# Kernel tuning notes

Hardware: AMD Instinct MI355X
Metric: run time of the kernel (lower is better)

Reference implementation:

```python
import math
import jax, jax.numpy as jnp
import numpy as np

HEAD_DIM = 64
N_HEAD = 8
INIT_SIZE = 1200  # -> 1201 embeddings, origin_shift = 601


def rel_sinusoidal_pos_embed(seq_len, dim=HEAD_DIM):
    """Matches RelativeSinusoidalPositionalEmbedding(dim, padding_idx=0, init_size=1200)."""
    num = INIT_SIZE + 1  # 1201
    half = dim // 2
    inv_freq = jnp.exp(jnp.arange(half, dtype=jnp.float32) * -(math.log(10000.0) / (half - 1)))
    pos = jnp.arange(-(num // 2), num // 2, dtype=jnp.float32)  # -601 .. 599 (1201 values)
    ang = pos[:, None] * inv_freq[None, :]                      # [num, half]
    w = jnp.concatenate([jnp.sin(ang), jnp.cos(ang)], axis=1)   # [num, dim]
    w = w.at[0].set(0.0)  # padding_idx row zeroed
    origin_shift = num // 2 + 1  # 601
    idx = jnp.arange(-seq_len, seq_len) + origin_shift          # [2L]
    return w[idx]                                               # [2L, dim]


def _shift(BD):
    # BD: [b, n, L, 2L] -> [b, n, L, L] (Transformer-XL skew trick)
    b, n, L, _ = BD.shape
    BD = jnp.pad(BD, ((0, 0), (0, 0), (0, 0), (0, 1)))  # [b,n,L,2L+1]
    BD = BD.reshape(b, n, 2 * L + 1, L)[:, :, :-1].reshape(b, n, L, 2 * L)
    return BD[:, :, :, L:]


def _transpose_shift(E):
    # E: [b, n, L, 2L] -> [b, n, L, L]
    b, n, L, _ = E.shape
    E = jnp.pad(E, ((0, 0), (0, 0), (0, 0), (0, 1))).reshape(b, n, 2 * L + 1, L)
    idx = jnp.arange(L) * 2 + 1
    return jnp.swapaxes(E[:, :, idx, :], -1, -2)


def setup_inputs() -> dict:
    key = jax.random.key(0)
    k1, k2, k3, k4 = jax.random.split(key, 4)
    B, L, D = 8, 512, 512
    x = jax.random.normal(k1, (B, L, D), dtype=jnp.float32)
    mask = jnp.ones((B, L), dtype=jnp.int32)
    W_qkv = jax.random.normal(k2, (D, 3 * D), dtype=jnp.float32) * (1.0 / math.sqrt(D))
    r_r_bias = jax.random.normal(k3, (N_HEAD, HEAD_DIM), dtype=jnp.float32) * 0.1
    r_w_bias = jax.random.normal(k4, (N_HEAD, HEAD_DIM), dtype=jnp.float32) * 0.1
    return {"x": x, "mask": mask, "W_qkv": W_qkv, "r_r_bias": r_r_bias, "r_w_bias": r_w_bias}


def reference(x, mask, W_qkv, r_r_bias, r_w_bias):
    B, L, D = x.shape
    scale = math.sqrt(HEAD_DIM)
    pos = rel_sinusoidal_pos_embed(L)  # [2L, head_dim], detached constant

    qkv = x @ W_qkv  # [B, L, 3D]
    q, k, v = jnp.split(qkv, 3, axis=-1)
    q = q.reshape(B, L, N_HEAD, HEAD_DIM).transpose(0, 2, 1, 3)  # [B,H,L,d]
    k = k.reshape(B, L, N_HEAD, HEAD_DIM).transpose(0, 2, 1, 3)
    v = v.reshape(B, L, N_HEAD, HEAD_DIM).transpose(0, 2, 1, 3)

    rw_head_q = q + r_r_bias[None, :, None, :]
    AC = jnp.einsum('bnqd,bnkd->bnqk', rw_head_q, k)              # [B,H,L,L]
    D_ = jnp.einsum('nd,ld->nl', r_w_bias, pos)[None, :, None, :] # [1,H,1,2L]
    B_ = jnp.einsum('bnqd,ld->bnql', q, pos)                      # [B,H,L,2L]
    E_ = jnp.einsum('bnqd,ld->bnql', k, pos)                      # [B,H,L,2L]

    BDE = _shift(B_ + D_) + _transpose_shift(E_)                  # [B,H,L,L]
    attn = (AC + BDE) / scale
    attn = jnp.where(mask[:, None, None, :] == 0, -jnp.inf, attn)
    attn = jax.nn.softmax(attn, axis=-1)

    out = jnp.matmul(attn, v)                                     # [B,H,L,d]
    return out.transpose(0, 2, 1, 3).reshape(B, L, D)
```

## Files before the change

kernel.cpp:

```cpp
#include <hip/hip_runtime.h>
#include <hip/hip_bf16.h>
#include <math.h>

#define LSEQ 512
#define DDIM 192

typedef __attribute__((ext_vector_type(8))) short s16x8;
typedef __attribute__((ext_vector_type(4))) float f32x4;
typedef unsigned short ushort_t;
typedef unsigned int uint_t;

#define MFMA16(a, b, c) __builtin_amdgcn_mfma_f32_16x16x32_bf16(a, b, c, 0, 0, 0)

__device__ __forceinline__ ushort_t f2b(float f) {
  union { float f; uint_t u; } v; v.f = f;
  uint_t r = (v.u + 0x7FFFu + ((v.u >> 16) & 1u)) >> 16;
  return (ushort_t)r;
}
__device__ __forceinline__ float b2f(ushort_t u) {
  union { uint_t u; float f; } v; v.u = ((uint_t)u) << 16;
  return v.f;
}

typedef const __attribute__((address_space(1))) void g_void_t;
typedef __attribute__((address_space(3))) void lds_void_t;
__device__ __forceinline__ void load_lds16(const void* g, void* l) {
  __builtin_amdgcn_global_load_lds((g_void_t*)g, (lds_void_t*)l, 16, 0, 0);
}

__device__ __forceinline__ size_t kswz(size_t row, int d) {
  return row * DDIM + (size_t)((d & 0x1C7) | ((((d >> 3) & 7) ^ ((int)row & 7)) << 3));
}

__global__ void cast_all(const float* __restrict__ x, const float* __restrict__ W,
                         ushort_t* __restrict__ xb, ushort_t* __restrict__ Wt) {
  __shared__ float tile[32][33];
  const int id = blockIdx.x;
  if (id < 1024) {
    const int i = (id * 256 + threadIdx.x) * 8;
    const int row = i >> 9, k = i & 511;
    float4 a = *(const float4*)(x + i);
    float4 b = *(const float4*)(x + i + 4);
    uint4 o;
    o.x = (uint_t)f2b(a.x) | ((uint_t)f2b(a.y) << 16);
    o.y = (uint_t)f2b(a.z) | ((uint_t)f2b(a.w) << 16);
    o.z = (uint_t)f2b(b.x) | ((uint_t)f2b(b.y) << 16);
    o.w = (uint_t)f2b(b.z) | ((uint_t)f2b(b.w) << 16);
    const int dst = row * 512 + (k & 448) + (((((k >> 3) & 7) ^ (row & 7))) << 3);
    *(uint4*)(xb + dst) = o;
  } else {
    const int wid = id - 1024;
    const int tx = threadIdx.x & 31, ty = threadIdx.x >> 5;
    const int k0 = (wid & 15) * 32, n0 = (wid >> 4) * 32;
#pragma unroll
    for (int i = 0; i < 4; ++i)
      tile[ty + i * 8][tx] = W[(size_t)(k0 + ty + i * 8) * 1536 + n0 + tx];
    __syncthreads();
#pragma unroll
    for (int i = 0; i < 4; ++i) {
      const int n = n0 + ty + i * 8, k = k0 + tx;
      Wt[(size_t)n * 512 + (k & 448) + ((((k >> 3) & 7) ^ (n & 7)) << 3) + (k & 7)] =
          f2b(tile[tx][ty + i * 8]);
    }
  }
}

__global__ __launch_bounds__(256, 2) void qkv_gemm(
    const ushort_t* __restrict__ xb, const ushort_t* __restrict__ Wt,
    const float* __restrict__ rr, const float* __restrict__ rw,
    ushort_t* __restrict__ Qt, ushort_t* __restrict__ Kt, ushort_t* __restrict__ Vt) {
  __shared__ __align__(16) ushort_t ldsA[2][128 * 64];
  __shared__ __align__(16) ushort_t ldsB[2][128 * 64];
  const int tid = threadIdx.x;
  const int w = tid >> 6, lane = tid & 63, lo = lane & 15, hi = lane >> 4;
  const int wm = w >> 1, wn = w & 1;
  const int id = blockIdx.x;
  const int mp = id & 31, np = id >> 5;
  const int m0 = mp * 128, n0 = np * 128;

  f32x4 acc[4][4];
  const f32x4 zero4 = {0.f, 0.f, 0.f, 0.f};
#pragma unroll
  for (int i = 0; i < 4; ++i)
#pragma unroll
    for (int j = 0; j < 4; ++j) acc[i][j] = zero4;

  const char* asrc = (const char*)xb + (size_t)m0 * 1024;
  const char* bsrc = (const char*)Wt + (size_t)n0 * 1024;

#define STAGE_QKV(buf, ks)                                                     \
  {                                                                            \
    char* la = (char*)&ldsA[buf][0];                                           \
    char* lb = (char*)&ldsB[buf][0];                                           \
    _Pragma("unroll") for (int it = 0; it < 4; ++it) {                         \
      const int X = it * 4096 + tid * 16;                                      \
      load_lds16(asrc + (size_t)(X >> 7) * 1024 + (ks) * 128 + (X & 127),      \
                 la + X);                                                      \
      load_lds16(bsrc + (size_t)(X >> 7) * 1024 + (ks) * 128 + (X & 127),      \
                 lb + X);                                                      \
    }                                                                          \
  }

  STAGE_QKV(0, 0);
  for (int ks = 0; ks < 8; ++ks) {
    const int cur = ks & 1;
    __syncthreads();
    if (ks < 7) STAGE_QKV(cur ^ 1, ks + 1);
    const char* Ab = (const char*)&ldsA[cur][0];
    const char* Bb = (const char*)&ldsB[cur][0];
#pragma unroll
    for (int kh = 0; kh < 2; ++kh) {
      const int sw = ((kh * 4 + hi) ^ (lo & 7)) << 4;
      s16x8 a[4], bf[4];
#pragma unroll
      for (int i = 0; i < 4; ++i)
        a[i] = *(const s16x8*)(Ab + (wm * 64 + i * 16 + lo) * 128 + sw);
#pragma unroll
      for (int j = 0; j < 4; ++j)
        bf[j] = *(const s16x8*)(Bb + (wn * 64 + j * 16 + lo) * 128 + sw);
#pragma unroll
      for (int i = 0; i < 4; ++i)
#pragma unroll
        for (int j = 0; j < 4; ++j)
          acc[i][j] = MFMA16(a[i], bf[j], acc[i][j]);
    }
  }

  const int gn0 = n0 + wn * 64;
  const int sect = gn0 >> 9;
  const int h = (gn0 >> 6) & 7;
  const int mrow0 = m0 + wm * 64;

  if (sect == 2) {
#pragma unroll
    for (int i = 0; i < 4; ++i) {
      const int m16 = mrow0 + i * 16;
      const int b = m16 >> 9;
      const int l0 = (m16 + hi * 4) & 511;
#pragma unroll
      for (int j = 0; j < 4; ++j) {
        ushort4 pk;
        pk.x = f2b(acc[i][j][0]); pk.y = f2b(acc[i][j][1]);
        pk.z = f2b(acc[i][j][2]); pk.w = f2b(acc[i][j][3]);
        *(ushort4*)&Vt[(((size_t)b * 8 + h) * 64 + j * 16 + lo) * 512 + l0] = pk;
      }
    }
  } else if (sect == 0) {
    float bias[4];
    int dcol[4];
#pragma unroll
    for (int j = 0; j < 4; ++j) {
      dcol[j] = (j < 2) ? j * 16 + lo : 32 + (j - 2) * 16 + lo;
      bias[j] = rr[h * 64 + dcol[j]];
    }
#pragma unroll
    for (int i = 0; i < 4; ++i)
#pragma unroll
      for (int r = 0; r < 4; ++r) {
        const int m = mrow0 + i * 16 + hi * 4 + r;
        const size_t row = ((size_t)(m >> 9) * 8 + h) * 512 + (m & 511);
#pragma unroll
        for (int j = 0; j < 4; ++j)
          Qt[row * 64 + dcol[j]] = f2b((acc[i][j][r] + bias[j]) * 0.125f);
      }
  } else {
#pragma unroll
    for (int p = 0; p < 2; ++p) {
      const int hf = p * 16 + lo;
      const float fq = __expf(-(float)hf * 0.29710775393472f);
      float sfr, cfr;
      __sincosf(fq, &sfr, &cfr);
#pragma unroll
      for (int i = 0; i < 4; ++i)
#pragma unroll
        for (int r = 0; r < 4; ++r) {
          const int m = mrow0 + i * 16 + hi * 4 + r;
          const int l = m & 511;
          const size_t row = ((size_t)(m >> 9) * 8 + h) * 512 + l;
          float s0, c0;
          __sincosf((float)l * fq, &s0, &c0);
          const float s1 = s0 * cfr + c0 * sfr;
          const float c1 = c0 * cfr - s0 * sfr;
          const float ks_ = acc[i][p][r], kc_ = acc[i][p + 2][r];
          Kt[kswz(row, hf)]       = f2b(ks_);
          Kt[kswz(row, 32 + hf)]  = f2b(kc_);
          Kt[kswz(row, 64 + hf)]  = f2b(s1);
          Kt[kswz(row, 96 + hf)]  = f2b(c1);
          Kt[kswz(row, 128 + hf)] = f2b(ks_ * c0 + kc_ * s0);
          Kt[kswz(row, 160 + hf)] = f2b(kc_ * c0 - ks_ * s0);
        }
    }
  }
}

__global__ __launch_bounds__(256, 2) void attn_kernel(
    const ushort_t* __restrict__ Qt, const ushort_t* __restrict__ Kt,
    const ushort_t* __restrict__ Vt, const int* __restrict__ mask,
    const float* __restrict__ rr, const float* __restrict__ rw,
    float* __restrict__ out) {
  __shared__ __align__(16) ushort_t ldsK[2][64 * DDIM];
  __shared__ __align__(16) ushort_t P[4][16][72];

  const int tid = threadIdx.x;
  const int w = tid >> 6;
  const int lane = tid & 63, lo = lane & 15, hi = lane >> 4;
  const int id = blockIdx.x;
  const int bh = id & 63, qg = id >> 6;
  const int b = bh >> 3, h = bh & 7;
  const int q0 = qg * 64 + w * 16;
  const size_t qrow0 = (size_t)bh * LSEQ + q0;

  s16x8 qf[6];
  {
    const ushort_t* qbase = Qt + (qrow0 + lo) * 64 + hi * 8;
    qf[0] = *(const s16x8*)(qbase);
    qf[1] = *(const s16x8*)(qbase + 32);
    const int l = q0 + lo;
#pragma unroll
    for (int j = 0; j < 8; ++j) {
      const int hfj = hi * 8 + j;
      const float fq = __expf(-(float)hfj * 0.29710775393472f);
      float s0, c0, s1, c1;
      __sincosf((float)l * fq, &s0, &c0);
      __sincosf((float)(l + 1) * fq, &s1, &c1);
      const float ds = 0.125f * (rw[h * 64 + hfj] - rr[h * 64 + hfj]);
      const float dc = 0.125f * (rw[h * 64 + 32 + hfj] - rr[h * 64 + 32 + hfj]);
      const float qs = b2f((ushort_t)qf[0][j]) + ds;
      const float qc = b2f((ushort_t)qf[1][j]) + dc;
      qf[2][j] = (short)f2b(qs * c0 + qc * s0);
      qf[3][j] = (short)f2b(qc * c0 - qs * s0);
      qf[4][j] = (short)f2b(0.125f * s1);
      qf[5][j] = (short)f2b(0.125f * c1);
    }
  }

  const f32x4 zero4 = {0.f, 0.f, 0.f, 0.f};
  f32x4 o[4];
#pragma unroll
  for (int j = 0; j < 4; ++j) o[j] = zero4;
  float mrun = -3.0e38f, lrun = 0.f;

  const char* ksrc = (const char*)(Kt + (size_t)bh * LSEQ * DDIM);
  const ushort_t* vbase = Vt + ((size_t)bh * 64 + lo) * 512 + hi * 8;

#pragma unroll
  for (int it = 0; it < 6; ++it) {
    const int X = it * 4096 + tid * 16;
    load_lds16(ksrc + X, (char*)&ldsK[0][0] + X);
  }

  for (int kt = 0; kt < 8; ++kt) {
    const int cur = kt & 1;

    const int mk = mask[b * LSEQ + kt * 64 + lane];
    s16x8 vbf[2][4];
#pragma unroll
    for (int kh = 0; kh < 2; ++kh)
#pragma unroll
      for (int j = 0; j < 4; ++j)
        vbf[kh][j] = *(const s16x8*)(vbase + (size_t)j * 16 * 512 + kt * 64 + kh * 32);

    asm volatile("s_waitcnt vmcnt(8)" ::: "memory");
    __builtin_amdgcn_s_barrier();
    __builtin_amdgcn_sched_barrier(0);

    if (kt < 7) {
      const char* s = ksrc + (kt + 1) * 24576;
      char* d = (char*)&ldsK[cur ^ 1][0];
#pragma unroll
      for (int it = 0; it < 6; ++it) {
        const int X = it * 4096 + tid * 16;
        load_lds16(s + X, d + X);
      }
    }

    f32x4 sf[4];
#pragma unroll
    for (int f = 0; f < 4; ++f) sf[f] = zero4;
    const char* kl = (const char*)&ldsK[cur][0];
    __builtin_amdgcn_s_setprio(1);
#pragma unroll
    for (int ks = 0; ks < 6; ++ks) {
      const int swb = ((ks * 4 + hi) ^ (lo & 7)) << 4;
#pragma unroll
      for (int f = 0; f < 4; ++f) {
        s16x8 ka = *(const s16x8*)(kl + (f * 16 + lo) * 384 + swb);
        sf[f] = MFMA16(ka, qf[ks], sf[f]);
      }
    }
    __builtin_amdgcn_s_setprio(0);

    if (__ballot(mk == 0) != 0ull) {
#pragma unroll
      for (int f = 0; f < 4; ++f)
#pragma unroll
        for (int r = 0; r < 4; ++r)
          if (__shfl(mk, f * 16 + hi * 4 + r) == 0) sf[f][r] = -3.0e38f;
    }

    float tm = fmaxf(fmaxf(sf[0][0], sf[0][1]), fmaxf(sf[0][2], sf[0][3]));
#pragma unroll
    for (int f = 1; f < 4; ++f)
      tm = fmaxf(tm, fmaxf(fmaxf(sf[f][0], sf[f][1]), fmaxf(sf[f][2], sf[f][3])));
    tm = fmaxf(tm, __shfl_xor(tm, 16));
    tm = fmaxf(tm, __shfl_xor(tm, 32));

    if (!__all(tm - mrun <= 8.0f)) {
      const float mnew = fmaxf(mrun, tm);
      const float corr = __expf(mrun - mnew);
      lrun *= corr;
      mrun = mnew;
      float cq[4];
#pragma unroll
      for (int r = 0; r < 4; ++r) cq[r] = __shfl(corr, hi * 4 + r);
#pragma unroll
      for (int j = 0; j < 4; ++j)
#pragma unroll
        for (int r = 0; r < 4; ++r) o[j][r] *= cq[r];
    }

    float ts = 0.f;
#pragma unroll
    for (int f = 0; f < 4; ++f)
#pragma unroll
      for (int r = 0; r < 4; ++r) {
        sf[f][r] = __expf(sf[f][r] - mrun);
        ts += sf[f][r];
      }
    ts += __shfl_xor(ts, 16);
    ts += __shfl_xor(ts, 32);
    lrun += ts;

#pragma unroll
    for (int f = 0; f < 4; ++f) {
      __hip_bfloat162 p0 = __float22bfloat162_rn(make_float2(sf[f][0], sf[f][1]));
      __hip_bfloat162 p1 = __float22bfloat162_rn(make_float2(sf[f][2], sf[f][3]));
      uint2 u;
      __builtin_memcpy(&u.x, &p0, 4);
      __builtin_memcpy(&u.y, &p1, 4);
      *(uint2*)&P[w][lo][f * 16 + hi * 4] = u;
    }

    __builtin_amdgcn_s_setprio(1);
#pragma unroll
    for (int kh = 0; kh < 2; ++kh) {
      s16x8 pa = *(const s16x8*)&P[w][lo][kh * 32 + hi * 8];
#pragma unroll
      for (int j = 0; j < 4; ++j)
        o[j] = MFMA16(pa, vbf[kh][j], o[j]);
    }
    __builtin_amdgcn_s_setprio(0);
  }

  float lq[4];
#pragma unroll
  for (int r = 0; r < 4; ++r) lq[r] = 1.0f / __shfl(lrun, hi * 4 + r);
#pragma unroll
  for (int j = 0; j < 4; ++j)
#pragma unroll
    for (int r = 0; r < 4; ++r)
      out[((size_t)b * LSEQ + q0 + hi * 4 + r) * 512 + h * 64 + j * 16 + lo] =
          o[j][r] * lq[r];
}

extern "C" void kernel_launch(void* const* d_in, const int* in_sizes, int n_in,
                              void* d_out, int out_size, void* d_ws, size_t ws_size,
                              hipStream_t stream) {
  const float* x    = (const float*)d_in[0];
  const int*   mask = (const int*)d_in[1];
  const float* W    = (const float*)d_in[2];
  const float* rr   = (const float*)d_in[3];
  const float* rw   = (const float*)d_in[4];
  float* out = (float*)d_out;

  char* ws = (char*)d_ws;
  ushort_t* xb = (ushort_t*)(ws);
  ushort_t* Wt = (ushort_t*)(ws + 4194304);
  ushort_t* Qt = (ushort_t*)(ws + 5767168);
  ushort_t* Kt = (ushort_t*)(ws + 9961472);
  ushort_t* Vt = (ushort_t*)(ws + 22544384);

  cast_all<<<1792, 256, 0, stream>>>(x, W, xb, Wt);
  qkv_gemm<<<384, 256, 0, stream>>>(xb, Wt, rr, rw, Qt, Kt, Vt);
  attn_kernel<<<512, 256, 0, stream>>>(Qt, Kt, Vt, mask, rr, rw, out);
}
```

Measured before the change: 51.33 us.

## Fuse fp32-to-bf16 cast of x into QKV GEMM staging via registers

The separate pass that converts x to bf16 and writes it to workspace is removed. The QKV GEMM now loads fp32 x tiles into registers, converts them with a packed bf16 conversion instruction, and writes them swizzled into LDS after the MFMA loop, while W still streams directly to LDS. Softmax probabilities also use the packed conversion instruction. This saves a global round trip and part of a launch, but the GEMM now reads twice as many bytes for A, uses more registers, and loses the asynchronous direct-to-LDS path for that operand.

```diff
diff --git a/kernel.cpp b/kernel.cpp
--- a/kernel.cpp
+++ b/kernel.cpp
@@ -21,6 +21,11 @@
   union { uint_t u; float f; } v; v.u = ((uint_t)u) << 16;
   return v.f;
 }
+__device__ __forceinline__ uint_t cvtpk(float a, float b) {
+  uint_t r;
+  asm("v_cvt_pk_bf16_f32 %0, %1, %2" : "=v"(r) : "v"(a), "v"(b));
+  return r;
+}
 
 typedef const __attribute__((address_space(1))) void g_void_t;
 typedef __attribute__((address_space(3))) void lds_void_t;
@@ -32,41 +37,25 @@
   return row * DDIM + (size_t)((d & 0x1C7) | ((((d >> 3) & 7) ^ ((int)row & 7)) << 3));
 }
 
-__global__ void cast_all(const float* __restrict__ x, const float* __restrict__ W,
-                         ushort_t* __restrict__ xb, ushort_t* __restrict__ Wt) {
+__global__ void cast_w(const float* __restrict__ W, ushort_t* __restrict__ Wt) {
   __shared__ float tile[32][33];
-  const int id = blockIdx.x;
-  if (id < 1024) {
-    const int i = (id * 256 + threadIdx.x) * 8;
-    const int row = i >> 9, k = i & 511;
-    float4 a = *(const float4*)(x + i);
-    float4 b = *(const float4*)(x + i + 4);
-    uint4 o;
-    o.x = (uint_t)f2b(a.x) | ((uint_t)f2b(a.y) << 16);
-    o.y = (uint_t)f2b(a.z) | ((uint_t)f2b(a.w) << 16);
-    o.z = (uint_t)f2b(b.x) | ((uint_t)f2b(b.y) << 16);
-    o.w = (uint_t)f2b(b.z) | ((uint_t)f2b(b.w) << 16);
-    const int dst = row * 512 + (k & 448) + (((((k >> 3) & 7) ^ (row & 7))) << 3);
-    *(uint4*)(xb + dst) = o;
-  } else {
-    const int wid = id - 1024;
-    const int tx = threadIdx.x & 31, ty = threadIdx.x >> 5;
-    const int k0 = (wid & 15) * 32, n0 = (wid >> 4) * 32;
-#pragma unroll
-    for (int i = 0; i < 4; ++i)
-      tile[ty + i * 8][tx] = W[(size_t)(k0 + ty + i * 8) * 1536 + n0 + tx];
-    __syncthreads();
-#pragma unroll
-    for (int i = 0; i < 4; ++i) {
-      const int n = n0 + ty + i * 8, k = k0 + tx;
-      Wt[(size_t)n * 512 + (k & 448) + ((((k >> 3) & 7) ^ (n & 7)) << 3) + (k & 7)] =
-          f2b(tile[tx][ty + i * 8]);
-    }
+  const int wid = blockIdx.x;
+  const int tx = threadIdx.x & 31, ty = threadIdx.x >> 5;
+  const int k0 = (wid & 15) * 32, n0 = (wid >> 4) * 32;
+#pragma unroll
+  for (int i = 0; i < 4; ++i)
+    tile[ty + i * 8][tx] = W[(size_t)(k0 + ty + i * 8) * 1536 + n0 + tx];
+  __syncthreads();
+#pragma unroll
+  for (int i = 0; i < 4; ++i) {
+    const int n = n0 + ty + i * 8, k = k0 + tx;
+    Wt[(size_t)n * 512 + (k & 448) + ((((k >> 3) & 7) ^ (n & 7)) << 3) + (k & 7)] =
+        f2b(tile[tx][ty + i * 8]);
   }
 }
 
 __global__ __launch_bounds__(256, 2) void qkv_gemm(
-    const ushort_t* __restrict__ xb, const ushort_t* __restrict__ Wt,
+    const float* __restrict__ x, const ushort_t* __restrict__ Wt,
     const float* __restrict__ rr, const float* __restrict__ rw,
     ushort_t* __restrict__ Qt, ushort_t* __restrict__ Kt, ushort_t* __restrict__ Vt) {
   __shared__ __align__(16) ushort_t ldsA[2][128 * 64];
@@ -85,27 +74,47 @@
 #pragma unroll
     for (int j = 0; j < 4; ++j) acc[i][j] = zero4;
 
-  const char* asrc = (const char*)xb + (size_t)m0 * 1024;
+  const float* axs = x + (size_t)m0 * 512;
   const char* bsrc = (const char*)Wt + (size_t)n0 * 1024;
-
-#define STAGE_QKV(buf, ks)                                                     \
-  {                                                                            \
-    char* la = (char*)&ldsA[buf][0];                                           \
-    char* lb = (char*)&ldsB[buf][0];                                           \
-    _Pragma("unroll") for (int it = 0; it < 4; ++it) {                         \
-      const int X = it * 4096 + tid * 16;                                      \
-      load_lds16(asrc + (size_t)(X >> 7) * 1024 + (ks) * 128 + (X & 127),      \
-                 la + X);                                                      \
-      load_lds16(bsrc + (size_t)(X >> 7) * 1024 + (ks) * 128 + (X & 127),      \
-                 lb + X);                                                      \
-    }                                                                          \
-  }
-
-  STAGE_QKV(0, 0);
+  const int arow = tid >> 3, akb = tid & 7;
+  float4 areg[4][2];
+
+#define LOADA_Q(ks)                                                            \
+  _Pragma("unroll") for (int it = 0; it < 4; ++it) {                           \
+    const float* p = axs + (size_t)(arow + it * 32) * 512 + (ks) * 64 + akb * 8; \
+    areg[it][0] = *(const float4*)p;                                           \
+    areg[it][1] = *(const float4*)(p + 4);                                     \
+  }
+
+#define WRITEA_Q(buf)                                                          \
+  _Pragma("unroll") for (int it = 0; it < 4; ++it) {                           \
+    const int row = arow + it * 32;                                            \
+    uint4 u;                                                                   \
+    u.x = cvtpk(areg[it][0].x, areg[it][0].y);                                 \
+    u.y = cvtpk(areg[it][0].z, areg[it][0].w);                                 \
+    u.z = cvtpk(areg[it][1].x, areg[it][1].y);                                 \
+    u.w = cvtpk(areg[it][1].z, areg[it][1].w);                                 \
+    *(uint4*)&ldsA[buf][row * 64 + ((akb ^ (row & 7)) << 3)] = u;              \
+  }
+
+#define STAGEB_Q(buf, ks)                                                      \
+  _Pragma("unroll") for (int it = 0; it < 4; ++it) {                           \
+    const int X = it * 4096 + tid * 16;                                        \
+    load_lds16(bsrc + (size_t)(X >> 7) * 1024 + (ks) * 128 + (X & 127),        \
+               (char*)&ldsB[buf][0] + X);                                      \
+  }
+
+  LOADA_Q(0);
+  STAGEB_Q(0, 0);
+  WRITEA_Q(0);
+
   for (int ks = 0; ks < 8; ++ks) {
     const int cur = ks & 1;
     __syncthreads();
-    if (ks < 7) STAGE_QKV(cur ^ 1, ks + 1);
+    if (ks < 7) {
+      LOADA_Q(ks + 1);
+      STAGEB_Q(cur ^ 1, ks + 1);
+    }
     const char* Ab = (const char*)&ldsA[cur][0];
     const char* Bb = (const char*)&ldsB[cur][0];
 #pragma unroll
@@ -124,6 +133,7 @@
         for (int j = 0; j < 4; ++j)
           acc[i][j] = MFMA16(a[i], bf[j], acc[i][j]);
     }
+    if (ks < 7) WRITEA_Q(cur ^ 1);
   }
 
   const int gn0 = n0 + wn * 64;
@@ -333,11 +343,9 @@
 
 #pragma unroll
     for (int f = 0; f < 4; ++f) {
-      __hip_bfloat162 p0 = __float22bfloat162_rn(make_float2(sf[f][0], sf[f][1]));
-      __hip_bfloat162 p1 = __float22bfloat162_rn(make_float2(sf[f][2], sf[f][3]));
       uint2 u;
-      __builtin_memcpy(&u.x, &p0, 4);
-      __builtin_memcpy(&u.y, &p1, 4);
+      u.x = cvtpk(sf[f][0], sf[f][1]);
+      u.y = cvtpk(sf[f][2], sf[f][3]);
       *(uint2*)&P[w][lo][f * 16 + hi * 4] = u;
     }
 
@@ -374,13 +382,12 @@
   float* out = (float*)d_out;
 
   char* ws = (char*)d_ws;
-  ushort_t* xb = (ushort_t*)(ws);
-  ushort_t* Wt = (ushort_t*)(ws + 4194304);
-  ushort_t* Qt = (ushort_t*)(ws + 5767168);
-  ushort_t* Kt = (ushort_t*)(ws + 9961472);
-  ushort_t* Vt = (ushort_t*)(ws + 22544384);
-
-  cast_all<<<1792, 256, 0, stream>>>(x, W, xb, Wt);
-  qkv_gemm<<<384, 256, 0, stream>>>(xb, Wt, rr, rw, Qt, Kt, Vt);
+  ushort_t* Wt = (ushort_t*)(ws);
+  ushort_t* Qt = (ushort_t*)(ws + 2097152);
+  ushort_t* Kt = (ushort_t*)(ws + 6291456);
+  ushort_t* Vt = (ushort_t*)(ws + 18874368);
+
+  cast_w<<<768, 256, 0, stream>>>(W, Wt);
+  qkv_gemm<<<384, 256, 0, stream>>>(x, Wt, rr, rw, Qt, Kt, Vt);
   attn_kernel<<<512, 256, 0, stream>>>(Qt, Kt, Vt, mask, rr, rw, out);
 }
```

Result: slower. 53.26 us (+3.8%).

## Fuse QKV GEMM and attention into one persistent kernel with per-head flags

Applied to the files above, without the earlier changes.

Merges the QKV projection GEMM and the attention kernel into a single launch. The first 384 blocks compute GEMM tiles and then increment per-(batch, head) atomic counters. Every block then spins until its head's Q/K/V tiles are ready before running attention. This removes a kernel launch boundary and lets attention for finished heads overlap with remaining GEMM work. It relies on all 512 blocks being co-resident (a deadlock risk otherwise) and adds spin-wait overhead. It also switches the P bf16 packing to an inline v_cvt_pk_bf16_f32 instruction.

```diff
diff --git a/kernel.cpp b/kernel.cpp
--- a/kernel.cpp
+++ b/kernel.cpp
@@ -21,6 +21,11 @@
   union { uint_t u; float f; } v; v.u = ((uint_t)u) << 16;
   return v.f;
 }
+__device__ __forceinline__ uint_t cvtpk(float a, float b) {
+  uint_t r;
+  asm("v_cvt_pk_bf16_f32 %0, %1, %2" : "=v"(r) : "v"(a), "v"(b));
+  return r;
+}
 
 typedef const __attribute__((address_space(1))) void g_void_t;
 typedef __attribute__((address_space(3))) void lds_void_t;
@@ -33,7 +38,8 @@
 }
 
 __global__ void cast_all(const float* __restrict__ x, const float* __restrict__ W,
-                         ushort_t* __restrict__ xb, ushort_t* __restrict__ Wt) {
+                         ushort_t* __restrict__ xb, ushort_t* __restrict__ Wt,
+                         uint_t* __restrict__ flags) {
   __shared__ float tile[32][33];
   const int id = blockIdx.x;
   if (id < 1024) {
@@ -50,6 +56,7 @@
     *(uint4*)(xb + dst) = o;
   } else {
     const int wid = id - 1024;
+    if (wid == 0 && threadIdx.x < 64) flags[threadIdx.x] = 0u;
     const int tx = threadIdx.x & 31, ty = threadIdx.x >> 5;
     const int k0 = (wid & 15) * 32, n0 = (wid >> 4) * 32;
 #pragma unroll
@@ -65,33 +72,38 @@
   }
 }
 
-__global__ __launch_bounds__(256, 2) void qkv_gemm(
+__global__ __launch_bounds__(256, 2) void fused(
     const ushort_t* __restrict__ xb, const ushort_t* __restrict__ Wt,
     const float* __restrict__ rr, const float* __restrict__ rw,
-    ushort_t* __restrict__ Qt, ushort_t* __restrict__ Kt, ushort_t* __restrict__ Vt) {
-  __shared__ __align__(16) ushort_t ldsA[2][128 * 64];
-  __shared__ __align__(16) ushort_t ldsB[2][128 * 64];
+    ushort_t* __restrict__ Qt, ushort_t* __restrict__ Kt, ushort_t* __restrict__ Vt,
+    const int* __restrict__ mask, float* __restrict__ out,
+    uint_t* __restrict__ flags) {
+  __shared__ __align__(16) char smem[65536];
   const int tid = threadIdx.x;
+  const int bid = blockIdx.x;
   const int w = tid >> 6, lane = tid & 63, lo = lane & 15, hi = lane >> 4;
-  const int wm = w >> 1, wn = w & 1;
-  const int id = blockIdx.x;
-  const int mp = id & 31, np = id >> 5;
-  const int m0 = mp * 128, n0 = np * 128;
-
-  f32x4 acc[4][4];
-  const f32x4 zero4 = {0.f, 0.f, 0.f, 0.f};
-#pragma unroll
-  for (int i = 0; i < 4; ++i)
-#pragma unroll
-    for (int j = 0; j < 4; ++j) acc[i][j] = zero4;
-
-  const char* asrc = (const char*)xb + (size_t)m0 * 1024;
-  const char* bsrc = (const char*)Wt + (size_t)n0 * 1024;
+
+  if (bid < 384) {
+    ushort_t* ldsA = (ushort_t*)smem;
+    ushort_t* ldsB = (ushort_t*)(smem + 32768);
+    const int wm = w >> 1, wn = w & 1;
+    const int mp = bid & 31, np = bid >> 5;
+    const int m0 = mp * 128, n0 = np * 128;
+
+    f32x4 acc[4][4];
+    const f32x4 zero4 = {0.f, 0.f, 0.f, 0.f};
+#pragma unroll
+    for (int i = 0; i < 4; ++i)
+#pragma unroll
+      for (int j = 0; j < 4; ++j) acc[i][j] = zero4;
+
+    const char* asrc = (const char*)xb + (size_t)m0 * 1024;
+    const char* bsrc = (const char*)Wt + (size_t)n0 * 1024;
 
 #define STAGE_QKV(buf, ks)                                                     \
   {                                                                            \
-    char* la = (char*)&ldsA[buf][0];                                           \
-    char* lb = (char*)&ldsB[buf][0];                                           \
+    char* la = (char*)ldsA + (buf) * 16384;                                    \
+    char* lb = (char*)ldsB + (buf) * 16384;                                    \
     _Pragma("unroll") for (int it = 0; it < 4; ++it) {                         \
       const int X = it * 4096 + tid * 16;                                      \
       load_lds16(asrc + (size_t)(X >> 7) * 1024 + (ks) * 128 + (X & 127),      \
@@ -101,266 +113,276 @@
     }                                                                          \
   }
 
-  STAGE_QKV(0, 0);
-  for (int ks = 0; ks < 8; ++ks) {
-    const int cur = ks & 1;
-    __syncthreads();
-    if (ks < 7) STAGE_QKV(cur ^ 1, ks + 1);
-    const char* Ab = (const char*)&ldsA[cur][0];
-    const char* Bb = (const char*)&ldsB[cur][0];
-#pragma unroll
-    for (int kh = 0; kh < 2; ++kh) {
-      const int sw = ((kh * 4 + hi) ^ (lo & 7)) << 4;
-      s16x8 a[4], bf[4];
-#pragma unroll
-      for (int i = 0; i < 4; ++i)
-        a[i] = *(const s16x8*)(Ab + (wm * 64 + i * 16 + lo) * 128 + sw);
-#pragma unroll
-      for (int j = 0; j < 4; ++j)
-        bf[j] = *(const s16x8*)(Bb + (wn * 64 + j * 16 + lo) * 128 + sw);
-#pragma unroll
-      for (int i = 0; i < 4; ++i)
+    STAGE_QKV(0, 0);
+    for (int ks = 0; ks < 8; ++ks) {
+      const int cur = ks & 1;
+      __syncthreads();
+      if (ks < 7) STAGE_QKV(cur ^ 1, ks + 1);
+      const char* Ab = (const char*)ldsA + cur * 16384;
+      const char* Bb = (const char*)ldsB + cur * 16384;
+#pragma unroll
+      for (int kh = 0; kh < 2; ++kh) {
+        const int sw = ((kh * 4 + hi) ^ (lo & 7)) << 4;
+        s16x8 a[4], bf[4];
+#pragma unroll
+        for (int i = 0; i < 4; ++i)
+          a[i] = *(const s16x8*)(Ab + (wm * 64 + i * 16 + lo) * 128 + sw);
 #pragma unroll
         for (int j = 0; j < 4; ++j)
-          acc[i][j] = MFMA16(a[i], bf[j], acc[i][j]);
-    }
-  }
-
-  const int gn0 = n0 + wn * 64;
-  const int sect = gn0 >> 9;
-  const int h = (gn0 >> 6) & 7;
-  const int mrow0 = m0 + wm * 64;
-
-  if (sect == 2) {
-#pragma unroll
-    for (int i = 0; i < 4; ++i) {
-      const int m16 = mrow0 + i * 16;
-      const int b = m16 >> 9;
-      const int l0 = (m16 + hi * 4) & 511;
+          bf[j] = *(const s16x8*)(Bb + (wn * 64 + j * 16 + lo) * 128 + sw);
+#pragma unroll
+        for (int i = 0; i < 4; ++i)
+#pragma unroll
+          for (int j = 0; j < 4; ++j)
+            acc[i][j] = MFMA16(a[i], bf[j], acc[i][j]);
+      }
+    }
+
+    const int gn0 = n0 + wn * 64;
+    const int sect = gn0 >> 9;
+    const int h = (gn0 >> 6) & 7;
+    const int mrow0 = m0 + wm * 64;
+
+    if (sect == 2) {
+#pragma unroll
+      for (int i = 0; i < 4; ++i) {
+        const int m16 = mrow0 + i * 16;
+        const int b = m16 >> 9;
+        const int l0 = (m16 + hi * 4) & 511;
+#pragma unroll
+        for (int j = 0; j < 4; ++j) {
+          ushort4 pk;
+          pk.x = f2b(acc[i][j][0]); pk.y = f2b(acc[i][j][1]);
+          pk.z = f2b(acc[i][j][2]); pk.w = f2b(acc[i][j][3]);
+          *(ushort4*)&Vt[(((size_t)b * 8 + h) * 64 + j * 16 + lo) * 512 + l0] = pk;
+        }
+      }
+    } else if (sect == 0) {
+      float bias[4];
+      int dcol[4];
 #pragma unroll
       for (int j = 0; j < 4; ++j) {
-        ushort4 pk;
-        pk.x = f2b(acc[i][j][0]); pk.y = f2b(acc[i][j][1]);
-        pk.z = f2b(acc[i][j][2]); pk.w = f2b(acc[i][j][3]);
-        *(ushort4*)&Vt[(((size_t)b * 8 + h) * 64 + j * 16 + lo) * 512 + l0] = pk;
-      }
-    }
-  } else if (sect == 0) {
-    float bias[4];
-    int dcol[4];
-#pragma unroll
-    for (int j = 0; j < 4; ++j) {
-      dcol[j] = (j < 2) ? j * 16 + lo : 32 + (j - 2) * 16 + lo;
-      bias[j] = rr[h * 64 + dcol[j]];
-    }
-#pragma unroll
-    for (int i = 0; i < 4; ++i)
-#pragma unroll
-      for (int r = 0; r < 4; ++r) {
-        const int m = mrow0 + i * 16 + hi * 4 + r;
-        const size_t row = ((size_t)(m >> 9) * 8 + h) * 512 + (m & 511);
-#pragma unroll
-        for (int j = 0; j < 4; ++j)
-          Qt[row * 64 + dcol[j]] = f2b((acc[i][j][r] + bias[j]) * 0.125f);
-      }
-  } else {
-#pragma unroll
-    for (int p = 0; p < 2; ++p) {
-      const int hf = p * 16 + lo;
-      const float fq = __expf(-(float)hf * 0.29710775393472f);
-      float sfr, cfr;
-      __sincosf(fq, &sfr, &cfr);
+        dcol[j] = (j < 2) ? j * 16 + lo : 32 + (j - 2) * 16 + lo;
+        bias[j] = rr[h * 64 + dcol[j]];
+      }
 #pragma unroll
       for (int i = 0; i < 4; ++i)
 #pragma unroll
         for (int r = 0; r < 4; ++r) {
           const int m = mrow0 + i * 16 + hi * 4 + r;
-          const int l = m & 511;
-          const size_t row = ((size_t)(m >> 9) * 8 + h) * 512 + l;
-          float s0, c0;
-          __sincosf((float)l * fq, &s0, &c0);
-          const float s1 = s0 * cfr + c0 * sfr;
-          const float c1 = c0 * cfr - s0 * sfr;
-          const float ks_ = acc[i][p][r], kc_ = acc[i][p + 2][r];
-          Kt[kswz(row, hf)]       = f2b(ks_);
-          Kt[kswz(row, 32 + hf)]  = f2b(kc_);
-          Kt[kswz(row, 64 + hf)]  = f2b(s1);
-          Kt[kswz(row, 96 + hf)]  = f2b(c1);
-          Kt[kswz(row, 128 + hf)] = f2b(ks_ * c0 + kc_ * s0);
-          Kt[kswz(row, 160 + hf)] = f2b(kc_ * c0 - ks_ * s0);
+          const size_t row = ((size_t)(m >> 9) * 8 + h) * 512 + (m & 511);
+#pragma unroll
+          for (int j = 0; j < 4; ++j)
+            Qt[row * 64 + dcol[j]] = f2b((acc[i][j][r] + bias[j]) * 0.125f);
         }
+    } else {
+#pragma unroll
+      for (int p = 0; p < 2; ++p) {
+        const int hf = p * 16 + lo;
+        const float fq = __expf(-(float)hf * 0.29710775393472f);
+        float sfr, cfr;
+        __sincosf(fq, &sfr, &cfr);
+#pragma unroll
+        for (int i = 0; i < 4; ++i)
+#pragma unroll
+          for (int r = 0; r < 4; ++r) {
+            const int m = mrow0 + i * 16 + hi * 4 + r;
+            const int l = m & 511;
+            const size_t row = ((size_t)(m >> 9) * 8 + h) * 512 + l;
+            float s0, c0;
+            __sincosf((float)l * fq, &s0, &c0);
+            const float s1 = s0 * cfr + c0 * sfr;
+            const float c1 = c0 * cfr - s0 * sfr;
+            const float ks_ = acc[i][p][r], kc_ = acc[i][p + 2][r];
+            Kt[kswz(row, hf)]       = f2b(ks_);
+            Kt[kswz(row, 32 + hf)]  = f2b(kc_);
+            Kt[kswz(row, 64 + hf)]  = f2b(s1);
+            Kt[kswz(row, 96 + hf)]  = f2b(c1);
+            Kt[kswz(row, 128 + hf)] = f2b(ks_ * c0 + kc_ * s0);
+            Kt[kswz(row, 160 + hf)] = f2b(kc_ * c0 - ks_ * s0);
+          }
+      }
+    }
+
+    __syncthreads();
+    if (tid == 0) {
+      __threadfence();
+      const int pb = (bid & 31) >> 2;
+      const int ph0 = 2 * ((bid >> 5) & 3);
+      __hip_atomic_fetch_add(&flags[pb * 8 + ph0], 1u, __ATOMIC_RELAXED,
+                             __HIP_MEMORY_SCOPE_AGENT);
+      __hip_atomic_fetch_add(&flags[pb * 8 + ph0 + 1], 1u, __ATOMIC_RELAXED,
+                             __HIP_MEMORY_SCOPE_AGENT);
     }
   }
-}
-
-__global__ __launch_bounds__(256, 2) void attn_kernel(
-    const ushort_t* __restrict__ Qt, const ushort_t* __restrict__ Kt,
-    const ushort_t* __restrict__ Vt, const int* __restrict__ mask,
-    const float* __restrict__ rr, const float* __restrict__ rw,
-    float* __restrict__ out) {
-  __shared__ __align__(16) ushort_t ldsK[2][64 * DDIM];
-  __shared__ __align__(16) ushort_t P[4][16][72];
-
-  const int tid = threadIdx.x;
-  const int w = tid >> 6;
-  const int lane = tid & 63, lo = lane & 15, hi = lane >> 4;
-  const int id = blockIdx.x;
-  const int bh = id & 63, qg = id >> 6;
-  const int b = bh >> 3, h = bh & 7;
-  const int q0 = qg * 64 + w * 16;
-  const size_t qrow0 = (size_t)bh * LSEQ + q0;
-
-  s16x8 qf[6];
+
   {
-    const ushort_t* qbase = Qt + (qrow0 + lo) * 64 + hi * 8;
-    qf[0] = *(const s16x8*)(qbase);
-    qf[1] = *(const s16x8*)(qbase + 32);
-    const int l = q0 + lo;
-#pragma unroll
-    for (int j = 0; j < 8; ++j) {
-      const int hfj = hi * 8 + j;
-      const float fq = __expf(-(float)hfj * 0.29710775393472f);
-      float s0, c0, s1, c1;
-      __sincosf((float)l * fq, &s0, &c0);
-      __sincosf((float)(l + 1) * fq, &s1, &c1);
-      const float ds = 0.125f * (rw[h * 64 + hfj] - rr[h * 64 + hfj]);
-      const float dc = 0.125f * (rw[h * 64 + 32 + hfj] - rr[h * 64 + 32 + hfj]);
-      const float qs = b2f((ushort_t)qf[0][j]) + ds;
-      const float qc = b2f((ushort_t)qf[1][j]) + dc;
-      qf[2][j] = (short)f2b(qs * c0 + qc * s0);
-      qf[3][j] = (short)f2b(qc * c0 - qs * s0);
-      qf[4][j] = (short)f2b(0.125f * s1);
-      qf[5][j] = (short)f2b(0.125f * c1);
-    }
+    ushort_t* ldsK = (ushort_t*)smem;
+    ushort_t (*P)[16][72] = (ushort_t(*)[16][72])(smem + 49152);
+
+    const int bh = bid & 63, qg = bid >> 6;
+    const int b = bh >> 3, h = bh & 7;
+    const int q0 = qg * 64 + w * 16;
+    const size_t qrow0 = (size_t)bh * LSEQ + q0;
+
+    if (tid == 0) {
+      while (__hip_atomic_load(&flags[bh], __ATOMIC_RELAXED,
+                               __HIP_MEMORY_SCOPE_AGENT) < 12u)
+        __builtin_amdgcn_s_sleep(4);
+      __threadfence();
+    }
+    __syncthreads();
+
+    s16x8 qf[6];
+    {
+      const ushort_t* qbase = Qt + (qrow0 + lo) * 64 + hi * 8;
+      qf[0] = *(const s16x8*)(qbase);
+      qf[1] = *(const s16x8*)(qbase + 32);
+      const int l = q0 + lo;
+#pragma unroll
+      for (int j = 0; j < 8; ++j) {
+        const int hfj = hi * 8 + j;
+        const float fq = __expf(-(float)hfj * 0.29710775393472f);
+        float s0, c0, s1, c1;
+        __sincosf((float)l * fq, &s0, &c0);
+        __sincosf((float)(l + 1) * fq, &s1, &c1);
+        const float ds = 0.125f * (rw[h * 64 + hfj] - rr[h * 64 + hfj]);
+        const float dc = 0.125f * (rw[h * 64 + 32 + hfj] - rr[h * 64 + 32 + hfj]);
+        const float qs = b2f((ushort_t)qf[0][j]) + ds;
+        const float qc = b2f((ushort_t)qf[1][j]) + dc;
+        qf[2][j] = (short)f2b(qs * c0 + qc * s0);
+        qf[3][j] = (short)f2b(qc * c0 - qs * s0);
+        qf[4][j] = (short)f2b(0.125f * s1);
+        qf[5][j] = (short)f2b(0.125f * c1);
+      }
+    }
+
+    const f32x4 zero4 = {0.f, 0.f, 0.f, 0.f};
+    f32x4 o[4];
+#pragma unroll
+    for (int j = 0; j < 4; ++j) o[j] = zero4;
+    float mrun = -3.0e38f, lrun = 0.f;
+
+    const char* ksrc = (const char*)(Kt + (size_t)bh * LSEQ * DDIM);
+    const ushort_t* vbase = Vt + ((size_t)bh * 64 + lo) * 512 + hi * 8;
+
+#pragma unroll
+    for (int it = 0; it < 6; ++it) {
+      const int X = it * 4096 + tid * 16;
+      load_lds16(ksrc + X, (char*)ldsK + X);
+    }
+
+    for (int kt = 0; kt < 8; ++kt) {
+      const int cur = kt & 1;
+
+      const int mk = mask[b * LSEQ + kt * 64 + lane];
+      s16x8 vbf[2][4];
+#pragma unroll
+      for (int kh = 0; kh < 2; ++kh)
+#pragma unroll
+        for (int j = 0; j < 4; ++j)
+          vbf[kh][j] = *(const s16x8*)(vbase + (size_t)j * 16 * 512 + kt * 64 + kh * 32);
+
+      asm volatile("s_waitcnt vmcnt(8)" ::: "memory");
+      __builtin_amdgcn_s_barrier();
+      __builtin_amdgcn_sched_barrier(0);
+
+      if (kt < 7) {
+        const char* s = ksrc + (kt + 1) * 24576;
+        char* d = (char*)ldsK + (cur ^ 1) * 24576;
+#pragma unroll
+        for (int it = 0; it < 6; ++it) {
+          const int X = it * 4096 + tid * 16;
+          load_lds16(s + X, d + X);
+        }
+      }
+
+      f32x4 sf[4];
+#pragma unroll
+      for (int f = 0; f < 4; ++f) sf[f] = zero4;
+      const char* kl = (const char*)ldsK + cur * 24576;
+      __builtin_amdgcn_s_setprio(1);
+#pragma unroll
+      for (int ks = 0; ks < 6; ++ks) {
+        const int swb = ((ks * 4 + hi) ^ (lo & 7)) << 4;
+#pragma unroll
+        for (int f = 0; f < 4; ++f) {
+          s16x8 ka = *(const s16x8*)(kl + (f * 16 + lo) * 384 + swb);
+          sf[f] = MFMA16(ka, qf[ks], sf[f]);
+        }
+      }
+      __builtin_amdgcn_s_setprio(0);
+
+      if (__ballot(mk == 0) != 0ull) {
+#pragma unroll
+        for (int f = 0; f < 4; ++f)
+#pragma unroll
+          for (int r = 0; r < 4; ++r)
+            if (__shfl(mk, f * 16 + hi * 4 + r) == 0) sf[f][r] = -3.0e38f;
+      }
+
+      float tm = fmaxf(fmaxf(sf[0][0], sf[0][1]), fmaxf(sf[0][2], sf[0][3]));
+#pragma unroll
+      for (int f = 1; f < 4; ++f)
+        tm = fmaxf(tm, fmaxf(fmaxf(sf[f][0], sf[f][1]), fmaxf(sf[f][2], sf[f][3])));
+      tm = fmaxf(tm, __shfl_xor(tm, 16));
+      tm = fmaxf(tm, __shfl_xor(tm, 32));
+
+      if (!__all(tm - mrun <= 8.0f)) {
+        const float mnew = fmaxf(mrun, tm);
+        const float corr = __expf(mrun - mnew);
+        lrun *= corr;
+        mrun = mnew;
+        float cq[4];
+#pragma unroll
+        for (int r = 0; r < 4; ++r) cq[r] = __shfl(corr, hi * 4 + r);
+#pragma unroll
+        for (int j = 0; j < 4; ++j)
+#pragma unroll
+          for (int r = 0; r < 4; ++r) o[j][r] *= cq[r];
+      }
+
+      float ts = 0.f;
+#pragma unroll
+      for (int f = 0; f < 4; ++f)
+#pragma unroll
+        for (int r = 0; r < 4; ++r) {
+          sf[f][r] = __expf(sf[f][r] - mrun);
+          ts += sf[f][r];
+        }
+      ts += __shfl_xor(ts, 16);
+      ts += __shfl_xor(ts, 32);
+      lrun += ts;
+
+#pragma unroll
+      for (int f = 0; f < 4; ++f) {
+        uint2 u;
+        u.x = cvtpk(sf[f][0], sf[f][1]);
+        u.y = cvtpk(sf[f][2], sf[f][3]);
+        *(uint2*)&P[w][lo][f * 16 + hi * 4] = u;
+      }
+
+      __builtin_amdgcn_s_setprio(1);
+#pragma unroll
+      for (int kh = 0; kh < 2; ++kh) {
+        s16x8 pa = *(const s16x8*)&P[w][lo][kh * 32 + hi * 8];
+#pragma unroll
+        for (int j = 0; j < 4; ++j)
+          o[j] = MFMA16(pa, vbf[kh][j], o[j]);
+      }
+      __builtin_amdgcn_s_setprio(0);
+    }
+
+    float lq[4];
+#pragma unroll
+    for (int r = 0; r < 4; ++r) lq[r] = 1.0f / __shfl(lrun, hi * 4 + r);
+#pragma unroll
+    for (int j = 0; j < 4; ++j)
+#pragma unroll
+      for (int r = 0; r < 4; ++r)
+        out[((size_t)b * LSEQ + q0 + hi * 4 + r) * 512 + h * 64 + j * 16 + lo] =
+            o[j][r] * lq[r];
   }
-
-  const f32x4 zero4 = {0.f, 0.f, 0.f, 0.f};
-  f32x4 o[4];
-#pragma unroll
-  for (int j = 0; j < 4; ++j) o[j] = zero4;
-  float mrun = -3.0e38f, lrun = 0.f;
-
-  const char* ksrc = (const char*)(Kt + (size_t)bh * LSEQ * DDIM);
-  const ushort_t* vbase = Vt + ((size_t)bh * 64 + lo) * 512 + hi * 8;
-
-#pragma unroll
-  for (int it = 0; it < 6; ++it) {
-    const int X = it * 4096 + tid * 16;
-    load_lds16(ksrc + X, (char*)&ldsK[0][0] + X);
-  }
-
-  for (int kt = 0; kt < 8; ++kt) {
-    const int cur = kt & 1;
-
-    const int mk = mask[b * LSEQ + kt * 64 + lane];
-    s16x8 vbf[2][4];
-#pragma unroll
-    for (int kh = 0; kh < 2; ++kh)
-#pragma unroll
-      for (int j = 0; j < 4; ++j)
-        vbf[kh][j] = *(const s16x8*)(vbase + (size_t)j * 16 * 512 + kt * 64 + kh * 32);
-
-    asm volatile("s_waitcnt vmcnt(8)" ::: "memory");
-    __builtin_amdgcn_s_barrier();
-    __builtin_amdgcn_sched_barrier(0);
-
-    if (kt < 7) {
-      const char* s = ksrc + (kt + 1) * 24576;
-      char* d = (char*)&ldsK[cur ^ 1][0];
-#pragma unroll
-      for (int it = 0; it < 6; ++it) {
-        const int X = it * 4096 + tid * 16;
-        load_lds16(s + X, d + X);
-      }
-    }
-
-    f32x4 sf[4];
-#pragma unroll
-    for (int f = 0; f < 4; ++f) sf[f] = zero4;
-    const char* kl = (const char*)&ldsK[cur][0];
-    __builtin_amdgcn_s_setprio(1);
-#pragma unroll
-    for (int ks = 0; ks < 6; ++ks) {
-      const int swb = ((ks * 4 + hi) ^ (lo & 7)) << 4;
-#pragma unroll
-      for (int f = 0; f < 4; ++f) {
-        s16x8 ka = *(const s16x8*)(kl + (f * 16 + lo) * 384 + swb);
-        sf[f] = MFMA16(ka, qf[ks], sf[f]);
-      }
-    }
-    __builtin_amdgcn_s_setprio(0);
-
-    if (__ballot(mk == 0) != 0ull) {
-#pragma unroll
-      for (int f = 0; f < 4; ++f)
-#pragma unroll
-        for (int r = 0; r < 4; ++r)
-          if (__shfl(mk, f * 16 + hi * 4 + r) == 0) sf[f][r] = -3.0e38f;
-    }
-
-    float tm = fmaxf(fmaxf(sf[0][0], sf[0][1]), fmaxf(sf[0][2], sf[0][3]));
-#pragma unroll
-    for (int f = 1; f < 4; ++f)
-      tm = fmaxf(tm, fmaxf(fmaxf(sf[f][0], sf[f][1]), fmaxf(sf[f][2], sf[f][3])));
-    tm = fmaxf(tm, __shfl_xor(tm, 16));
-    tm = fmaxf(tm, __shfl_xor(tm, 32));
-
-    if (!__all(tm - mrun <= 8.0f)) {
-      const float mnew = fmaxf(mrun, tm);
-      const float corr = __expf(mrun - mnew);
-      lrun *= corr;
-      mrun = mnew;
-      float cq[4];
-#pragma unroll
-      for (int r = 0; r < 4; ++r) cq[r] = __shfl(corr, hi * 4 + r);
-#pragma unroll
-      for (int j = 0; j < 4; ++j)
-#pragma unroll
-        for (int r = 0; r < 4; ++r) o[j][r] *= cq[r];
-    }
-
-    float ts = 0.f;
-#pragma unroll
-    for (int f = 0; f < 4; ++f)
-#pragma unroll
-      for (int r = 0; r < 4; ++r) {
-        sf[f][r] = __expf(sf[f][r] - mrun);
-        ts += sf[f][r];
-      }
-    ts += __shfl_xor(ts, 16);
-    ts += __shfl_xor(ts, 32);
-    lrun += ts;
-
-#pragma unroll
-    for (int f = 0; f < 4; ++f) {
-      __hip_bfloat162 p0 = __float22bfloat162_rn(make_float2(sf[f][0], sf[f][1]));
-      __hip_bfloat162 p1 = __float22bfloat162_rn(make_float2(sf[f][2], sf[f][3]));
-      uint2 u;
-      __builtin_memcpy(&u.x, &p0, 4);
-      __builtin_memcpy(&u.y, &p1, 4);
-      *(uint2*)&P[w][lo][f * 16 + hi * 4] = u;
-    }
-
-    __builtin_amdgcn_s_setprio(1);
-#pragma unroll
-    for (int kh = 0; kh < 2; ++kh) {
-      s16x8 pa = *(const s16x8*)&P[w][lo][kh * 32 + hi * 8];
-#pragma unroll
-      for (int j = 0; j < 4; ++j)
-        o[j] = MFMA16(pa, vbf[kh][j], o[j]);
-    }
-    __builtin_amdgcn_s_setprio(0);
-  }
-
-  float lq[4];
-#pragma unroll
-  for (int r = 0; r < 4; ++r) lq[r] = 1.0f / __shfl(lrun, hi * 4 + r);
-#pragma unroll
-  for (int j = 0; j < 4; ++j)
-#pragma unroll
-    for (int r = 0; r < 4; ++r)
-      out[((size_t)b * LSEQ + q0 + hi * 4 + r) * 512 + h * 64 + j * 16 + lo] =
-          o[j][r] * lq[r];
 }
 
 extern "C" void kernel_launch(void* const* d_in, const int* in_sizes, int n_in,
@@ -379,8 +401,8 @@
   ushort_t* Qt = (ushort_t*)(ws + 5767168);
   ushort_t* Kt = (ushort_t*)(ws + 9961472);
   ushort_t* Vt = (ushort_t*)(ws + 22544384);
-
-  cast_all<<<1792, 256, 0, stream>>>(x, W, xb, Wt);
-  qkv_gemm<<<384, 256, 0, stream>>>(xb, Wt, rr, rw, Qt, Kt, Vt);
-  attn_kernel<<<512, 256, 0, stream>>>(Qt, Kt, Vt, mask, rr, rw, out);
-}
+  uint_t* flags = (uint_t*)(ws + 26738688);
+
+  cast_all<<<1792, 256, 0, stream>>>(x, W, xb, Wt, flags);
+  fused<<<512, 256, 0, stream>>>(xb, Wt, rr, rw, Qt, Kt, Vt, mask, out, flags);
+}
```

Measured after the change: 89.05 us. 73.5% more time.
